# Kernel optimization log

Hardware: AMD Instinct MI355X
Metric: run time of the kernel (lower is better)

The kernel has to match this reference:

```python
import jax, jax.numpy as jnp
import numpy as np

N_BINS = 20  # matches ECELoss_DRL(n_bins=20)


def setup_inputs() -> dict:
    key = jax.random.key(0)
    k1, k2 = jax.random.split(key)
    N, C = 1_000_000, 128
    logits = jax.random.normal(k1, (N, C), dtype=jnp.float32)
    softmaxes = jax.nn.softmax(logits, axis=-1)  # valid probabilities in (0,1]
    labels = jax.random.randint(k2, (N,), 0, C, dtype=jnp.int32)
    return {"softmaxes": softmaxes, "labels": labels}


def reference(softmaxes, labels):
    # torch.max(softmaxes, 1) -> (confidences, predictions)
    conf = jnp.max(softmaxes, axis=1)                  # [N]
    pred = jnp.argmax(softmaxes, axis=1)               # [N]
    acc = (pred == labels).astype(jnp.float32)         # [N]
    n = softmaxes.shape[0]

    # Bin b covers (b/n_bins, (b+1)/n_bins] -> single-pass bucketize replacing
    # the 20-iteration python loop of gt/le masks.
    bin_idx = jnp.clip(jnp.ceil(conf * N_BINS).astype(jnp.int32) - 1, 0, N_BINS - 1)

    ones = jnp.ones_like(conf)
    counts = jax.ops.segment_sum(ones, bin_idx, num_segments=N_BINS)    # [20]
    conf_sum = jax.ops.segment_sum(conf, bin_idx, num_segments=N_BINS)  # [20]
    acc_sum = jax.ops.segment_sum(acc, bin_idx, num_segments=N_BINS)    # [20]

    nonempty = counts > 0
    safe = jnp.maximum(counts, 1.0)
    avg_conf = conf_sum / safe
    avg_acc = acc_sum / safe
    prop = counts / n  # prop_in_bin = in_bin.float().mean()

    ece = jnp.sum(jnp.where(nonempty, jnp.abs(avg_conf - avg_acc) * prop, 0.0)).reshape(1)
    ys = jnp.where(nonempty, avg_acc, 0.0)  # per-bin accuracies, 0 for empty bins
    return ece, ys
```

## Files before the change

### kernel.cpp

```cpp
#include <hip/hip_runtime.h>

#define NBINS 20
#define C 128

typedef float vf4 __attribute__((ext_vector_type(4)));


__global__ __launch_bounds__(256) void ece_pass1(
    const float* __restrict__ sm, const int* __restrict__ labels, int N,
    double* __restrict__ g_csum, unsigned* __restrict__ g_cnt,
    unsigned* __restrict__ g_cor) {
  __shared__ float s_csum[NBINS];
  __shared__ unsigned s_cc[NBINS];
  const int tid = threadIdx.x;
  if (tid < NBINS) { s_csum[tid] = 0.f; s_cc[tid] = 0u; }
  __syncthreads();

  const int lane = tid & 63;
  const int p = lane & 7;
  const int r = lane >> 3;

  const long long gw   = (long long)blockIdx.x * 4 + (tid >> 6);
  const long long hstr = (long long)gridDim.x * 4 * 2;
  const long long nh   = ((long long)N + 7) >> 3;

  vf4 va[4], vb[4];
  int la = 0, lb = 0;

  auto issue = [&](long long hh, vf4 (&v)[4], int& lab) {
    const long long row = hh * 8 + r;
    if (row < (long long)N) {
      const vf4* rp = (const vf4*)(sm + row * (long long)C);
#pragma unroll
      for (int k = 0; k < 4; ++k)
        v[k] = __builtin_nontemporal_load(rp + p + k * 8);
      lab = labels[row];
    } else {
#pragma unroll
      for (int k = 0; k < 4; ++k) v[k] = (vf4){-2.f, -2.f, -2.f, -2.f};
      lab = -1;
    }
  };

  auto process = [&](long long hh, const vf4 (&v)[4], int lab) {
    float bv = -3.f;
    int bi = 0;
#pragma unroll
    for (int k = 0; k < 4; ++k) {
      const vf4 q = v[k];
      const int b0 = k * 32 + p * 4;
      if (q.x > bv) { bv = q.x; bi = b0; }
      if (q.y > bv) { bv = q.y; bi = b0 + 1; }
      if (q.z > bv) { bv = q.z; bi = b0 + 2; }
      if (q.w > bv) { bv = q.w; bi = b0 + 3; }
    }
#pragma unroll
    for (int off = 1; off <= 4; off <<= 1) {
      const float ov = __shfl_xor(bv, off);
      const int   oi = __shfl_xor(bi, off);
      if (ov > bv || (ov == bv && oi < bi)) { bv = ov; bi = oi; }
    }
    const long long row = hh * 8 + r;
    if (p == 0 && row < (long long)N) {
      int bin = (int)ceilf(bv * 20.0f) - 1;
      bin = min(max(bin, 0), NBINS - 1);
      atomicAdd(&s_csum[bin], bv);
      atomicAdd(&s_cc[bin], 1u + ((bi == lab) ? 0x10000u : 0u));
    }
  };

  long long h = gw * 2;
  long long hn = h + 1;
  issue(h, va, la);

  while (h < nh) {
    issue(hn, vb, lb);
    process(h, va, la);
    h = hn;
    hn = (h & 1) ? (h + hstr - 1) : (h + 1);
    if (h >= nh) break;
    issue(hn, va, la);
    process(h, vb, lb);
    h = hn;
    hn = (h & 1) ? (h + hstr - 1) : (h + 1);
  }

  __syncthreads();
  if (tid < NBINS) {
    const unsigned cc = s_cc[tid];
    if (cc) {
      atomicAdd(&g_cnt[tid], cc & 0xFFFFu);
      atomicAdd(&g_cor[tid], cc >> 16);
      atomicAdd(&g_csum[tid], (double)s_csum[tid]);
    }
  }
}

__global__ void ece_pass2(const double* __restrict__ g_csum,
                          const unsigned* __restrict__ g_cnt,
                          const unsigned* __restrict__ g_cor,
                          float* __restrict__ out, int N) {
  const int i = threadIdx.x;
  double contrib = 0.0;
  if (i < NBINS) {
    const unsigned c = g_cnt[i];
    const double safe = c ? (double)c : 1.0;
    const double avg_conf = g_csum[i] / safe;
    const double avg_acc  = (double)g_cor[i] / safe;
    out[1 + i] = c ? (float)avg_acc : 0.f;
    if (c) contrib = fabs(avg_conf - avg_acc) * ((double)c / (double)N);
  }
#pragma unroll
  for (int off = 16; off >= 1; off >>= 1) contrib += __shfl_down(contrib, off);
  if (i == 0) out[0] = (float)contrib;
}

extern "C" void kernel_launch(void* const* d_in, const int* in_sizes, int n_in,
                              void* d_out, int out_size, void* d_ws, size_t ws_size,
                              hipStream_t stream) {
  const float* sm     = (const float*)d_in[0];
  const int*   labels = (const int*)d_in[1];
  const int N = in_sizes[1];

  double*   g_csum = (double*)d_ws;
  unsigned* g_cnt  = (unsigned*)((char*)d_ws + NBINS * sizeof(double));
  unsigned* g_cor  = g_cnt + NBINS;

  (void)hipMemsetAsync(d_ws, 0,
                       NBINS * sizeof(double) + 2 * NBINS * sizeof(unsigned),
                       stream);

  ece_pass1<<<2048, 256, 0, stream>>>(sm, labels, N, g_csum, g_cnt, g_cor);
  ece_pass2<<<1, 64, 0, stream>>>(g_csum, g_cnt, g_cor, (float*)d_out, N);
}
```

Before: 626.4 us.

## Use contiguous per-block row ranges and per-block partials instead of global atomics

Each block now handles one contiguous range of rows, with its four waves striding through it, replacing the grid-strided pair-of-chunks traversal. Blocks write their per-bin partial sums and counts to workspace rather than doing global atomics, and a 640-thread final kernel reduces all block partials. This drops the memset launch and contention on the global float64 atomics. In exchange, each block streams one long contiguous region, which may change DRAM access locality, and the finalize kernel does more work.

```diff
diff --git a/kernel.cpp b/kernel.cpp
--- a/kernel.cpp
+++ b/kernel.cpp
@@ -2,14 +2,14 @@
 
 #define NBINS 20
 #define C 128
+#define BLOCKS 2048
 
 typedef float vf4 __attribute__((ext_vector_type(4)));
 
 
 __global__ __launch_bounds__(256) void ece_pass1(
     const float* __restrict__ sm, const int* __restrict__ labels, int N,
-    double* __restrict__ g_csum, unsigned* __restrict__ g_cnt,
-    unsigned* __restrict__ g_cor) {
+    float* __restrict__ bcsum, unsigned* __restrict__ bcc) {
   __shared__ float s_csum[NBINS];
   __shared__ unsigned s_cc[NBINS];
   const int tid = threadIdx.x;
@@ -19,17 +19,18 @@
   const int lane = tid & 63;
   const int p = lane & 7;
   const int r = lane >> 3;
+  const int w = tid >> 6;
 
-  const long long gw   = (long long)blockIdx.x * 4 + (tid >> 6);
-  const long long hstr = (long long)gridDim.x * 4 * 2;
-  const long long nh   = ((long long)N + 7) >> 3;
+  const long long rpb = ((long long)N + BLOCKS - 1) / BLOCKS;
+  const long long lo  = (long long)blockIdx.x * rpb;
+  const long long hi  = min(lo + rpb, (long long)N);
 
   vf4 va[4], vb[4];
   int la = 0, lb = 0;
 
-  auto issue = [&](long long hh, vf4 (&v)[4], int& lab) {
-    const long long row = hh * 8 + r;
-    if (row < (long long)N) {
+  auto issue = [&](long long rb, vf4 (&v)[4], int& lab) {
+    const long long row = rb + r;
+    if (row < hi) {
       const vf4* rp = (const vf4*)(sm + row * (long long)C);
 #pragma unroll
       for (int k = 0; k < 4; ++k)
@@ -42,7 +43,7 @@
     }
   };
 
-  auto process = [&](long long hh, const vf4 (&v)[4], int lab) {
+  auto process = [&](long long rb, const vf4 (&v)[4], int lab) {
     float bv = -3.f;
     int bi = 0;
 #pragma unroll
@@ -60,8 +61,8 @@
       const int   oi = __shfl_xor(bi, off);
       if (ov > bv || (ov == bv && oi < bi)) { bv = ov; bi = oi; }
     }
-    const long long row = hh * 8 + r;
-    if (p == 0 && row < (long long)N) {
+    const long long row = rb + r;
+    if (p == 0 && row < hi) {
       int bin = (int)ceilf(bv * 20.0f) - 1;
       bin = min(max(bin, 0), NBINS - 1);
       atomicAdd(&s_csum[bin], bv);
@@ -69,50 +70,71 @@
     }
   };
 
-  long long h = gw * 2;
-  long long hn = h + 1;
-  issue(h, va, la);
-
-  while (h < nh) {
-    issue(hn, vb, lb);
-    process(h, va, la);
-    h = hn;
-    hn = (h & 1) ? (h + hstr - 1) : (h + 1);
-    if (h >= nh) break;
-    issue(hn, va, la);
-    process(h, vb, lb);
-    h = hn;
-    hn = (h & 1) ? (h + hstr - 1) : (h + 1);
+  long long rb = lo + (long long)w * 8;
+  if (rb < hi) {
+    issue(rb, va, la);
+    while (true) {
+      long long rn = rb + 32;
+      if (rn < hi) issue(rn, vb, lb);
+      process(rb, va, la);
+      rb = rn;
+      if (rb >= hi) break;
+      rn = rb + 32;
+      if (rn < hi) issue(rn, va, la);
+      process(rb, vb, lb);
+      rb = rn;
+      if (rb >= hi) break;
+    }
   }
 
   __syncthreads();
   if (tid < NBINS) {
-    const unsigned cc = s_cc[tid];
-    if (cc) {
-      atomicAdd(&g_cnt[tid], cc & 0xFFFFu);
-      atomicAdd(&g_cor[tid], cc >> 16);
-      atomicAdd(&g_csum[tid], (double)s_csum[tid]);
-    }
+    bcsum[blockIdx.x * NBINS + tid] = s_csum[tid];
+    bcc[blockIdx.x * NBINS + tid]   = s_cc[tid];
   }
 }
 
-__global__ void ece_pass2(const double* __restrict__ g_csum,
-                          const unsigned* __restrict__ g_cnt,
-                          const unsigned* __restrict__ g_cor,
+__global__ void ece_pass2(const float* __restrict__ bcsum,
+                          const unsigned* __restrict__ bcc,
                           float* __restrict__ out, int N) {
-  const int i = threadIdx.x;
+  __shared__ double  sc[32][NBINS];
+  __shared__ unsigned scnt[32][NBINS];
+  __shared__ unsigned scor[32][NBINS];
+  const int t = threadIdx.x;
+  const int bin = t % NBINS;
+  const int chunk = t / NBINS;
+  double cs = 0.0;
+  unsigned cn = 0, co = 0;
+  for (int b = chunk; b < BLOCKS; b += 32) {
+    cs += (double)bcsum[b * NBINS + bin];
+    const unsigned cc = bcc[b * NBINS + bin];
+    cn += cc & 0xFFFFu;
+    co += cc >> 16;
+  }
+  sc[chunk][bin] = cs;
+  scnt[chunk][bin] = cn;
+  scor[chunk][bin] = co;
+  __syncthreads();
+
   double contrib = 0.0;
-  if (i < NBINS) {
-    const unsigned c = g_cnt[i];
-    const double safe = c ? (double)c : 1.0;
-    const double avg_conf = g_csum[i] / safe;
-    const double avg_acc  = (double)g_cor[i] / safe;
-    out[1 + i] = c ? (float)avg_acc : 0.f;
-    if (c) contrib = fabs(avg_conf - avg_acc) * ((double)c / (double)N);
+  if (t < NBINS) {
+    double csum = 0.0;
+    unsigned cnt = 0, cor = 0;
+#pragma unroll
+    for (int g = 0; g < 32; ++g) {
+      csum += sc[g][t];
+      cnt += scnt[g][t];
+      cor += scor[g][t];
+    }
+    const double safe = cnt ? (double)cnt : 1.0;
+    const double avg_conf = csum / safe;
+    const double avg_acc  = (double)cor / safe;
+    out[1 + t] = cnt ? (float)avg_acc : 0.f;
+    if (cnt) contrib = fabs(avg_conf - avg_acc) * ((double)cnt / (double)N);
   }
 #pragma unroll
   for (int off = 16; off >= 1; off >>= 1) contrib += __shfl_down(contrib, off);
-  if (i == 0) out[0] = (float)contrib;
+  if (t == 0) out[0] = (float)contrib;
 }
 
 extern "C" void kernel_launch(void* const* d_in, const int* in_sizes, int n_in,
@@ -122,14 +144,9 @@
   const int*   labels = (const int*)d_in[1];
   const int N = in_sizes[1];
 
-  double*   g_csum = (double*)d_ws;
-  unsigned* g_cnt  = (unsigned*)((char*)d_ws + NBINS * sizeof(double));
-  unsigned* g_cor  = g_cnt + NBINS;
+  float*    bcsum = (float*)d_ws;
+  unsigned* bcc   = (unsigned*)((char*)d_ws + BLOCKS * NBINS * sizeof(float));
 
-  (void)hipMemsetAsync(d_ws, 0,
-                       NBINS * sizeof(double) + 2 * NBINS * sizeof(unsigned),
-                       stream);
-
-  ece_pass1<<<2048, 256, 0, stream>>>(sm, labels, N, g_csum, g_cnt, g_cor);
-  ece_pass2<<<1, 64, 0, stream>>>(g_csum, g_cnt, g_cor, (float*)d_out, N);
+  ece_pass1<<<BLOCKS, 256, 0, stream>>>(sm, labels, N, bcsum, bcc);
+  ece_pass2<<<1, 640, 0, stream>>>(bcsum, bcc, (float*)d_out, N);
 }
```

New measurement: 646.2 us. 3.1% more time.
